# Kernel tuning notes

Hardware: AMD Instinct MI355X
Metric: run time of the kernel (lower is better)

The kernel has to match this reference:

```python
import jax, jax.numpy as jnp
import numpy as np

N_NODES = 50000


def _gcn_conv(x, src, dst, W, b, num_nodes):
    """PyG GCNConv: out = D^{-1/2}(A+I)D^{-1/2} (x @ W) + b, self-loops added."""
    h = x @ W  # [N, out]
    # degrees over edges incl. self-loops (src/dst already include self-loops)
    ones = jnp.ones(src.shape[0], dtype=h.dtype)
    deg = jax.ops.segment_sum(ones, dst, num_segments=num_nodes)
    dinv = jnp.where(deg > 0, jax.lax.rsqrt(deg), 0.0)
    norm = dinv[src] * dinv[dst]  # [E]
    msgs = h[src] * norm[:, None]  # [E, out] gather (memory-bound)
    out = jax.ops.segment_sum(msgs, dst, num_segments=num_nodes)
    return out + b


def setup_inputs() -> dict:
    key = jax.random.key(0)
    ks = jax.random.split(key, 8)
    in_c, h2, h1, out_c = 256, 256, 128, 128
    x = jax.random.normal(ks[0], (N_NODES, in_c), dtype=jnp.float32)
    edge_index = jax.random.randint(ks[1], (2, 800000), 0, N_NODES, dtype=jnp.int64)
    def glorot(k, fi, fo):
        s = float(np.sqrt(6.0 / (fi + fo)))
        return jax.random.uniform(k, (fi, fo), jnp.float32, -s, s)
    return {
        "x": x,
        "edge_index": edge_index,
        "W1": glorot(ks[2], in_c, h2), "b1": jnp.zeros((h2,), jnp.float32),
        "W2": glorot(ks[3], h2, h1), "b2": jnp.zeros((h1,), jnp.float32),
        "W3": glorot(ks[4], h1, out_c), "b3": jnp.zeros((out_c,), jnp.float32),
    }


def reference(x, edge_index, W1, b1, W2, b2, W3, b3):
    n = x.shape[0]
    loops = jnp.arange(n, dtype=edge_index.dtype)
    src = jnp.concatenate([edge_index[0], loops])
    dst = jnp.concatenate([edge_index[1], loops])
    # dropout is a no-op in eval mode (training=False)
    h1 = jax.nn.relu(_gcn_conv(x, src, dst, W1, b1, n))
    h2 = jax.nn.relu(_gcn_conv(h1, src, dst, W2, b2, n))
    h3 = jax.nn.relu(_gcn_conv(h2, src, dst, W3, b3, n))
    return jnp.concatenate([h1, h2, h3], axis=1)
```

## Files before the change

kernel.cpp:

```cpp
#include <hip/hip_runtime.h>

typedef __attribute__((ext_vector_type(8))) short bfrag8;
typedef __attribute__((ext_vector_type(4))) float f32x4v;

__device__ inline short f2bf(float f) {
    unsigned u = __builtin_bit_cast(unsigned, f);
    u = (u + 0x7FFFu + ((u >> 16) & 1u)) >> 16;
    return (short)u;
}
__device__ inline float bf2f(short s) {
    unsigned u = ((unsigned)(unsigned short)s) << 16;
    return __builtin_bit_cast(float, u);
}
__device__ inline int pack2(short lo, short hi) {
    return (int)(((unsigned)(unsigned short)lo) | (((unsigned)(unsigned short)hi) << 16));
}
__device__ inline int pad32i(int v) { return (v + 31) & ~31; }


__global__ void deg_count_kernel(const int* __restrict__ dst, int E, int* __restrict__ deg) {
    int e = blockIdx.x * blockDim.x + threadIdx.x;
    if (e < E) atomicAdd(&deg[dst[e]], 1);
}

__global__ void block_sum_kernel(const int* __restrict__ deg, int n, int* __restrict__ bsums) {
    int i = blockIdx.x * 256 + threadIdx.x;
    int v = (i < n) ? pad32i(deg[i] + 1) : 0;
#pragma unroll
    for (int off = 32; off > 0; off >>= 1) v += __shfl_down(v, off);
    __shared__ int wsum[4];
    int lane = threadIdx.x & 63, w = threadIdx.x >> 6;
    if (lane == 0) wsum[w] = v;
    __syncthreads();
    if (threadIdx.x == 0) bsums[blockIdx.x] = wsum[0] + wsum[1] + wsum[2] + wsum[3];
}

__global__ void scan_bsums_kernel(int* __restrict__ bsums, int B, int* __restrict__ offs, int n) {
    __shared__ int s[256];
    int tid = threadIdx.x;
    int v = (tid < B) ? bsums[tid] : 0;
    s[tid] = v;
    __syncthreads();
    for (int off = 1; off < 256; off <<= 1) {
        int t = (tid >= off) ? s[tid - off] : 0;
        __syncthreads();
        s[tid] += t;
        __syncthreads();
    }
    if (tid < B) bsums[tid] = (tid == 0) ? 0 : s[tid - 1];
    if (tid == 0) offs[n] = s[255];
}

__global__ void scan_final_kernel(const int* __restrict__ deg, int n,
                                  const int* __restrict__ bsums,
                                  int* __restrict__ offs, int* __restrict__ cursor,
                                  float* __restrict__ dinv, int* __restrict__ csr) {
    __shared__ int s[256];
    int tid = threadIdx.x;
    int i = blockIdx.x * 256 + tid;
    int vt = (i < n) ? deg[i] + 1 : 0;
    int pv = (i < n) ? pad32i(vt) : 0;
    s[tid] = pv;
    __syncthreads();
    for (int off = 1; off < 256; off <<= 1) {
        int t = (tid >= off) ? s[tid - off] : 0;
        __syncthreads();
        s[tid] += t;
        __syncthreads();
    }
    if (i < n) {
        int excl = s[tid] - pv + bsums[blockIdx.x];
        offs[i] = excl;
        csr[excl] = i;
        cursor[i] = excl + 1;
        for (int p = excl + vt; p < excl + pv; ++p) csr[p] = n;
        dinv[i] = rsqrtf((float)vt);
    }
}

__global__ void csr_fill_kernel(const int* __restrict__ src, const int* __restrict__ dst, int E,
                                int* __restrict__ cursor, int* __restrict__ csr) {
    int e = blockIdx.x * blockDim.x + threadIdx.x;
    if (e < E) {
        int d = dst[e];
        int p = atomicAdd(&cursor[d], 1);
        csr[p] = src[e];
    }
}


__global__ void prep_kernel(const float* __restrict__ x, short* __restrict__ xb,
                            int total8, int totalp8,
                            const float* __restrict__ W1, short* __restrict__ Wt1,
                            const float* __restrict__ W2, short* __restrict__ Wt2,
                            const float* __restrict__ W3, short* __restrict__ Wt3) {
    int i = blockIdx.x * blockDim.x + threadIdx.x;
    if (i < total8) {
        const float4* p = (const float4*)(x + (size_t)i * 8);
        float4 v0 = p[0], v1 = p[1];
        int4 w = make_int4(pack2(f2bf(v0.x), f2bf(v0.y)), pack2(f2bf(v0.z), f2bf(v0.w)),
                           pack2(f2bf(v1.x), f2bf(v1.y)), pack2(f2bf(v1.z), f2bf(v1.w)));
        *(int4*)(xb + (size_t)i * 8) = w;
    } else if (i < totalp8) {
        *(int4*)(xb + (size_t)i * 8) = make_int4(0, 0, 0, 0);
    } else {
        int j = i - totalp8;
        if (j < 65536) {
            int k = j >> 8, c = j & 255;
            Wt1[c * 256 + k] = f2bf(W1[j]);
        } else if (j < 65536 + 32768) {
            int m = j - 65536;
            int k = m >> 7, c = m & 127;
            Wt2[c * 256 + k] = f2bf(W2[m]);
        } else if (j < 65536 + 32768 + 16384) {
            int m = j - 65536 - 32768;
            int k = m >> 7, c = m & 127;
            Wt3[c * 128 + k] = f2bf(W3[m]);
        }
    }
}


template<int K>
__global__ __launch_bounds__(256, 2) void gemm_skinny_kernel(
        const short* __restrict__ A,
        const short* __restrict__ Bt,
        const float* __restrict__ dinv,
        short* __restrict__ Tout, int ldt) {
    __shared__ short Bs[128 * K];
    char* bsb = (char*)Bs;

    const int tid = threadIdx.x;
    const int lane = tid & 63;
    const int wid = tid >> 6;
    const int l15 = lane & 15;
    const int quad = lane >> 4;
    const int q8 = quad * 8;
    const int bn = blockIdx.y * 128;
    const int row0 = blockIdx.x * 256 + wid * 64;

    {
        constexpr int TOT16 = 128 * K / 8;
#pragma unroll
        for (int i = tid; i < TOT16; i += 256) {
            int r = i / (K / 8);
            int c = (i % (K / 8)) * 8;
            int byte = (r * K + c) * 2;
            byte ^= (r & 7) << 4;
            *(int4*)(bsb + byte) = *(const int4*)&Bt[(size_t)(bn + r) * K + c];
        }
    }
    __syncthreads();

    f32x4v acc[4][8];
#pragma unroll
    for (int i = 0; i < 4; ++i)
#pragma unroll
        for (int j = 0; j < 8; ++j) acc[i][j] = (f32x4v){0.f, 0.f, 0.f, 0.f};

    const short* aBase = A + (size_t)(row0 + l15) * K + q8;

#pragma unroll
    for (int ks = 0; ks < K / 32; ++ks) {
        bfrag8 af[4], bf[8];
#pragma unroll
        for (int mt = 0; mt < 4; ++mt)
            af[mt] = *(const bfrag8*)(aBase + (size_t)mt * 16 * K + ks * 32);
#pragma unroll
        for (int nt = 0; nt < 8; ++nt) {
            int r = nt * 16 + l15;
            int byte = (r * K + ks * 32 + q8) * 2;
            byte ^= (r & 7) << 4;
            bf[nt] = *(const bfrag8*)(bsb + byte);
        }
#pragma unroll
        for (int mt = 0; mt < 4; ++mt)
#pragma unroll
            for (int nt = 0; nt < 8; ++nt)
                acc[mt][nt] = __builtin_amdgcn_mfma_f32_16x16x32_bf16(af[mt], bf[nt], acc[mt][nt], 0, 0, 0);
    }

#pragma unroll
    for (int mt = 0; mt < 4; ++mt) {
#pragma unroll
        for (int r = 0; r < 4; ++r) {
            int grow = row0 + mt * 16 + quad * 4 + r;
            float di = dinv[grow];
            short* outp = Tout + (size_t)grow * ldt + bn + l15;
#pragma unroll
            for (int nt = 0; nt < 8; ++nt)
                outp[nt * 16] = f2bf(acc[mt][nt][r] * di);
        }
    }
}


template<bool WB>
__global__ __launch_bounds__(256) void agg256_kernel(
        const short* __restrict__ hn, const float* __restrict__ dinv,
        const int* __restrict__ offs, const int* __restrict__ csr,
        const float* __restrict__ bias, float* __restrict__ out,
        short* __restrict__ hb, int coloff, int n) {
    int node = blockIdx.x * 4 + (threadIdx.x >> 6);
    if (node >= n) return;
    int lane = threadIdx.x & 63;
    int hl = lane & 31;
    int sub = lane >> 5;
    const short* base = hn + hl * 8;

    float acc[8];
#pragma unroll
    for (int v = 0; v < 8; ++v) acc[v] = 0.f;

    int beg = offs[node], end = offs[node + 1];
    for (int e = beg + sub; e < end; e += 16) {
        int s[8];
#pragma unroll
        for (int j = 0; j < 8; ++j) s[j] = csr[e + 2 * j];
        bfrag8 r[8];
#pragma unroll
        for (int j = 0; j < 8; ++j) r[j] = *(const bfrag8*)(base + (size_t)s[j] * 256);
#pragma unroll
        for (int j = 0; j < 8; ++j)
#pragma unroll
            for (int v = 0; v < 8; ++v) acc[v] += bf2f(r[j][v]);
    }

#pragma unroll
    for (int v = 0; v < 8; ++v) acc[v] += __shfl_xor(acc[v], 32);

    if (sub == 0) {
        float di = dinv[node];
        float res[8];
#pragma unroll
        for (int v = 0; v < 8; ++v)
            res[v] = fmaxf(fmaf(di, acc[v], bias[hl * 8 + v]), 0.f);
        float4* op = (float4*)(out + (size_t)node * 512 + coloff + hl * 8);
        op[0] = make_float4(res[0], res[1], res[2], res[3]);
        op[1] = make_float4(res[4], res[5], res[6], res[7]);
        if (WB) {
            int4 w = make_int4(pack2(f2bf(res[0]), f2bf(res[1])), pack2(f2bf(res[2]), f2bf(res[3])),
                               pack2(f2bf(res[4]), f2bf(res[5])), pack2(f2bf(res[6]), f2bf(res[7])));
            *(int4*)(hb + (size_t)node * 256 + hl * 8) = w;
        }
    }
}


template<bool WB>
__global__ __launch_bounds__(256) void agg128_kernel(
        const short* __restrict__ hn, const float* __restrict__ dinv,
        const int* __restrict__ offs, const int* __restrict__ csr,
        const float* __restrict__ bias, float* __restrict__ out,
        short* __restrict__ hb, int coloff, int n) {
    int node = blockIdx.x * 4 + (threadIdx.x >> 6);
    if (node >= n) return;
    int lane = threadIdx.x & 63;
    int ch = lane & 15;
    int sub = lane >> 4;
    const short* base = hn + ch * 8;

    float acc[8];
#pragma unroll
    for (int v = 0; v < 8; ++v) acc[v] = 0.f;

    int beg = offs[node], end = offs[node + 1];
    for (int e = beg + sub; e < end; e += 32) {
        int s[8];
#pragma unroll
        for (int j = 0; j < 8; ++j) s[j] = csr[e + 4 * j];
        bfrag8 r[8];
#pragma unroll
        for (int j = 0; j < 8; ++j) r[j] = *(const bfrag8*)(base + (size_t)s[j] * 128);
#pragma unroll
        for (int j = 0; j < 8; ++j)
#pragma unroll
            for (int v = 0; v < 8; ++v) acc[v] += bf2f(r[j][v]);
    }

#pragma unroll
    for (int v = 0; v < 8; ++v) {
        acc[v] += __shfl_xor(acc[v], 16);
        acc[v] += __shfl_xor(acc[v], 32);
    }

    if (sub == 0) {
        float di = dinv[node];
        float res[8];
#pragma unroll
        for (int v = 0; v < 8; ++v)
            res[v] = fmaxf(fmaf(di, acc[v], bias[ch * 8 + v]), 0.f);
        float4* op = (float4*)(out + (size_t)node * 512 + coloff + ch * 8);
        op[0] = make_float4(res[0], res[1], res[2], res[3]);
        op[1] = make_float4(res[4], res[5], res[6], res[7]);
        if (WB) {
            int4 w = make_int4(pack2(f2bf(res[0]), f2bf(res[1])), pack2(f2bf(res[2]), f2bf(res[3])),
                               pack2(f2bf(res[4]), f2bf(res[5])), pack2(f2bf(res[6]), f2bf(res[7])));
            *(int4*)(hb + (size_t)node * 128 + ch * 8) = w;
        }
    }
}


extern "C" void kernel_launch(void* const* d_in, const int* in_sizes, int n_in,
                              void* d_out, int out_size, void* d_ws, size_t ws_size,
                              hipStream_t stream) {
    const float* x  = (const float*)d_in[0];
    const int*   ei = (const int*)d_in[1];
    const float* W1 = (const float*)d_in[2];
    const float* b1 = (const float*)d_in[3];
    const float* W2 = (const float*)d_in[4];
    const float* b2 = (const float*)d_in[5];
    const float* W3 = (const float*)d_in[6];
    const float* b3 = (const float*)d_in[7];

    const int IN_C = 256, H2 = 256, H1 = 128, OUT_C = 128;
    int n = in_sizes[0] / IN_C;
    int E = in_sizes[1] / 2;
    const int* src = ei;
    const int* dst = ei + E;

    int sb = (n + 255) / 256;
    int npad = sb * 256;

    char* ws = (char*)d_ws;
    auto carve = [&](size_t bytes) { char* p = ws; ws += (bytes + 255) & ~(size_t)255; return p; };
    int*   deg    = (int*)  carve((size_t)n * 4);
    int*   offs   = (int*)  carve(((size_t)n + 1) * 4);
    int*   cursor = (int*)  carve((size_t)n * 4);
    float* dinv   = (float*)carve((size_t)npad * 4);
    int*   csr    = (int*)  carve(((size_t)E + 32 * (size_t)n) * 4);
    int*   bsums  = (int*)  carve(256 * 4);
    short* Wt1    = (short*)carve((size_t)IN_C * H2 * 2);
    short* Wt2    = (short*)carve((size_t)H2 * H1 * 2);
    short* Wt3    = (short*)carve((size_t)H1 * OUT_C * 2);
    short* t      = (short*)carve((size_t)npad * 256 * 2);
    short* inb    = (short*)carve((size_t)npad * 256 * 2);

    float* out = (float*)d_out;
    int nblk = (n + 255) / 256;

    hipMemsetAsync(deg, 0, (size_t)n * sizeof(int), stream);
    deg_count_kernel<<<(E + 255) / 256, 256, 0, stream>>>(dst, E, deg);
    block_sum_kernel<<<nblk, 256, 0, stream>>>(deg, n, bsums);
    scan_bsums_kernel<<<1, 256, 0, stream>>>(bsums, nblk, offs, n);
    scan_final_kernel<<<nblk, 256, 0, stream>>>(deg, n, bsums, offs, cursor, dinv, csr);
    csr_fill_kernel<<<(E + 255) / 256, 256, 0, stream>>>(src, dst, E, cursor, csr);

    int total8 = n * IN_C / 8;
    int totalp8 = npad * IN_C / 8;
    int prepTot = totalp8 + 65536 + 32768 + 16384;
    prep_kernel<<<(prepTot + 255) / 256, 256, 0, stream>>>(
        x, inb, total8, totalp8, W1, Wt1, W2, Wt2, W3, Wt3);

    gemm_skinny_kernel<256><<<dim3(sb, H2 / 128), 256, 0, stream>>>(inb, Wt1, dinv, t, H2);
    agg256_kernel<true><<<(n + 3) / 4, 256, 0, stream>>>(t, dinv, offs, csr, b1, out, inb, 0, n);

    gemm_skinny_kernel<256><<<dim3(sb, H1 / 128), 256, 0, stream>>>(inb, Wt2, dinv, t, H1);
    agg128_kernel<true><<<(n + 3) / 4, 256, 0, stream>>>(t, dinv, offs, csr, b2, out, inb, H2, n);

    hipMemsetAsync(inb + (size_t)n * 128, 0, (size_t)(npad - n) * 128 * 2, stream);

    gemm_skinny_kernel<128><<<dim3(sb, OUT_C / 128), 256, 0, stream>>>(inb, Wt3, dinv, t, OUT_C);
    agg128_kernel<false><<<(n + 3) / 4, 256, 0, stream>>>(t, dinv, offs, csr, b3, out, nullptr, H2 + H1, n);
}
```

Measured before the change: 425.5 us.

## Halve CSR row padding, vectorize atomics, fuse scans, add nontemporal memory ops

CSR rows are now padded to multiples of 16 instead of 32. This cuts the dummy gathers in aggregation, and agg128 gets a half-width tail iteration to cover rows that are not multiples of 32. The degree-count and CSR-fill kernels each process four edges per thread with int4 loads. The block-sum scan is folded into scan_final so one launch disappears. The separate padding memset is replaced by having agg128 zero the padded rows. Index loads and output stores now use nontemporal hints, which may change cache behaviour for data that is reused.

```diff
diff --git a/kernel.cpp b/kernel.cpp
--- a/kernel.cpp
+++ b/kernel.cpp
@@ -2,6 +2,7 @@
 
 typedef __attribute__((ext_vector_type(8))) short bfrag8;
 typedef __attribute__((ext_vector_type(4))) float f32x4v;
+typedef __attribute__((ext_vector_type(4))) int   i32x4v;
 
 __device__ inline short f2bf(float f) {
     unsigned u = __builtin_bit_cast(unsigned, f);
@@ -15,17 +16,23 @@
 __device__ inline int pack2(short lo, short hi) {
     return (int)(((unsigned)(unsigned short)lo) | (((unsigned)(unsigned short)hi) << 16));
 }
-__device__ inline int pad32i(int v) { return (v + 31) & ~31; }
+__device__ inline int pad16i(int v) { return (v + 15) & ~15; }
 
 
 __global__ void deg_count_kernel(const int* __restrict__ dst, int E, int* __restrict__ deg) {
-    int e = blockIdx.x * blockDim.x + threadIdx.x;
-    if (e < E) atomicAdd(&deg[dst[e]], 1);
+    int e = (blockIdx.x * blockDim.x + threadIdx.x) * 4;
+    if (e + 3 < E) {
+        int4 d = *(const int4*)(dst + e);
+        atomicAdd(&deg[d.x], 1); atomicAdd(&deg[d.y], 1);
+        atomicAdd(&deg[d.z], 1); atomicAdd(&deg[d.w], 1);
+    } else {
+        for (; e < E; ++e) atomicAdd(&deg[dst[e]], 1);
+    }
 }
 
 __global__ void block_sum_kernel(const int* __restrict__ deg, int n, int* __restrict__ bsums) {
     int i = blockIdx.x * 256 + threadIdx.x;
-    int v = (i < n) ? pad32i(deg[i] + 1) : 0;
+    int v = (i < n) ? pad16i(deg[i] + 1) : 0;
 #pragma unroll
     for (int off = 32; off > 0; off >>= 1) v += __shfl_down(v, off);
     __shared__ int wsum[4];
@@ -35,31 +42,26 @@
     if (threadIdx.x == 0) bsums[blockIdx.x] = wsum[0] + wsum[1] + wsum[2] + wsum[3];
 }
 
-__global__ void scan_bsums_kernel(int* __restrict__ bsums, int B, int* __restrict__ offs, int n) {
-    __shared__ int s[256];
-    int tid = threadIdx.x;
-    int v = (tid < B) ? bsums[tid] : 0;
-    s[tid] = v;
-    __syncthreads();
-    for (int off = 1; off < 256; off <<= 1) {
-        int t = (tid >= off) ? s[tid - off] : 0;
-        __syncthreads();
-        s[tid] += t;
-        __syncthreads();
-    }
-    if (tid < B) bsums[tid] = (tid == 0) ? 0 : s[tid - 1];
-    if (tid == 0) offs[n] = s[255];
-}
-
-__global__ void scan_final_kernel(const int* __restrict__ deg, int n,
+__global__ void scan_final_kernel(const int* __restrict__ deg, int n, int B,
                                   const int* __restrict__ bsums,
                                   int* __restrict__ offs, int* __restrict__ cursor,
                                   float* __restrict__ dinv, int* __restrict__ csr) {
+    __shared__ int sb[256];
     __shared__ int s[256];
     int tid = threadIdx.x;
+    sb[tid] = (tid < B) ? bsums[tid] : 0;
+    __syncthreads();
+    for (int off = 1; off < 256; off <<= 1) {
+        int t = (tid >= off) ? sb[tid - off] : 0;
+        __syncthreads();
+        sb[tid] += t;
+        __syncthreads();
+    }
+    int myBase = (blockIdx.x == 0) ? 0 : sb[blockIdx.x - 1];
+    int total = sb[255];
     int i = blockIdx.x * 256 + tid;
     int vt = (i < n) ? deg[i] + 1 : 0;
-    int pv = (i < n) ? pad32i(vt) : 0;
+    int pv = (i < n) ? pad16i(vt) : 0;
     s[tid] = pv;
     __syncthreads();
     for (int off = 1; off < 256; off <<= 1) {
@@ -69,22 +71,35 @@
         __syncthreads();
     }
     if (i < n) {
-        int excl = s[tid] - pv + bsums[blockIdx.x];
+        int excl = s[tid] - pv + myBase;
         offs[i] = excl;
         csr[excl] = i;
         cursor[i] = excl + 1;
         for (int p = excl + vt; p < excl + pv; ++p) csr[p] = n;
         dinv[i] = rsqrtf((float)vt);
-    }
+    } else if (i < gridDim.x * 256) {
+        dinv[i] = 0.f;
+    }
+    if (blockIdx.x == 0 && tid == 0) offs[n] = total;
 }
 
 __global__ void csr_fill_kernel(const int* __restrict__ src, const int* __restrict__ dst, int E,
                                 int* __restrict__ cursor, int* __restrict__ csr) {
-    int e = blockIdx.x * blockDim.x + threadIdx.x;
-    if (e < E) {
-        int d = dst[e];
-        int p = atomicAdd(&cursor[d], 1);
-        csr[p] = src[e];
+    int e = (blockIdx.x * blockDim.x + threadIdx.x) * 4;
+    if (e + 3 < E) {
+        int4 s4 = *(const int4*)(src + e);
+        int4 d4 = *(const int4*)(dst + e);
+        int p;
+        p = atomicAdd(&cursor[d4.x], 1); __builtin_nontemporal_store(s4.x, csr + p);
+        p = atomicAdd(&cursor[d4.y], 1); __builtin_nontemporal_store(s4.y, csr + p);
+        p = atomicAdd(&cursor[d4.z], 1); __builtin_nontemporal_store(s4.z, csr + p);
+        p = atomicAdd(&cursor[d4.w], 1); __builtin_nontemporal_store(s4.w, csr + p);
+    } else {
+        for (; e < E; ++e) {
+            int d = dst[e];
+            int p = atomicAdd(&cursor[d], 1);
+            __builtin_nontemporal_store(src[e], csr + p);
+        }
     }
 }
 
@@ -216,7 +231,7 @@
     for (int e = beg + sub; e < end; e += 16) {
         int s[8];
 #pragma unroll
-        for (int j = 0; j < 8; ++j) s[j] = csr[e + 2 * j];
+        for (int j = 0; j < 8; ++j) s[j] = __builtin_nontemporal_load(csr + e + 2 * j);
         bfrag8 r[8];
 #pragma unroll
         for (int j = 0; j < 8; ++j) r[j] = *(const bfrag8*)(base + (size_t)s[j] * 256);
@@ -235,13 +250,15 @@
 #pragma unroll
         for (int v = 0; v < 8; ++v)
             res[v] = fmaxf(fmaf(di, acc[v], bias[hl * 8 + v]), 0.f);
-        float4* op = (float4*)(out + (size_t)node * 512 + coloff + hl * 8);
-        op[0] = make_float4(res[0], res[1], res[2], res[3]);
-        op[1] = make_float4(res[4], res[5], res[6], res[7]);
+        float* op = out + (size_t)node * 512 + coloff + hl * 8;
+        f32x4v w0 = {res[0], res[1], res[2], res[3]};
+        f32x4v w1 = {res[4], res[5], res[6], res[7]};
+        __builtin_nontemporal_store(w0, (f32x4v*)op);
+        __builtin_nontemporal_store(w1, (f32x4v*)(op + 4));
         if (WB) {
-            int4 w = make_int4(pack2(f2bf(res[0]), f2bf(res[1])), pack2(f2bf(res[2]), f2bf(res[3])),
-                               pack2(f2bf(res[4]), f2bf(res[5])), pack2(f2bf(res[6]), f2bf(res[7])));
-            *(int4*)(hb + (size_t)node * 256 + hl * 8) = w;
+            i32x4v w = {pack2(f2bf(res[0]), f2bf(res[1])), pack2(f2bf(res[2]), f2bf(res[3])),
+                        pack2(f2bf(res[4]), f2bf(res[5])), pack2(f2bf(res[6]), f2bf(res[7]))};
+            __builtin_nontemporal_store(w, (i32x4v*)(hb + (size_t)node * 256 + hl * 8));
         }
     }
 }
@@ -252,10 +269,13 @@
         const short* __restrict__ hn, const float* __restrict__ dinv,
         const int* __restrict__ offs, const int* __restrict__ csr,
         const float* __restrict__ bias, float* __restrict__ out,
-        short* __restrict__ hb, int coloff, int n) {
+        short* __restrict__ hb, int coloff, int n, int npad) {
     int node = blockIdx.x * 4 + (threadIdx.x >> 6);
-    if (node >= n) return;
     int lane = threadIdx.x & 63;
+    if (node >= n) {
+        if (WB && node < npad) ((int*)(hb + (size_t)node * 128))[lane] = 0;
+        return;
+    }
     int ch = lane & 15;
     int sub = lane >> 4;
     const short* base = hn + ch * 8;
@@ -265,15 +285,28 @@
     for (int v = 0; v < 8; ++v) acc[v] = 0.f;
 
     int beg = offs[node], end = offs[node + 1];
-    for (int e = beg + sub; e < end; e += 32) {
+    int e = beg + sub;
+    for (; e + 16 < end; e += 32) {
         int s[8];
 #pragma unroll
-        for (int j = 0; j < 8; ++j) s[j] = csr[e + 4 * j];
+        for (int j = 0; j < 8; ++j) s[j] = __builtin_nontemporal_load(csr + e + 4 * j);
         bfrag8 r[8];
 #pragma unroll
         for (int j = 0; j < 8; ++j) r[j] = *(const bfrag8*)(base + (size_t)s[j] * 128);
 #pragma unroll
         for (int j = 0; j < 8; ++j)
+#pragma unroll
+            for (int v = 0; v < 8; ++v) acc[v] += bf2f(r[j][v]);
+    }
+    if (e < end) {
+        int s[4];
+#pragma unroll
+        for (int j = 0; j < 4; ++j) s[j] = __builtin_nontemporal_load(csr + e + 4 * j);
+        bfrag8 r[4];
+#pragma unroll
+        for (int j = 0; j < 4; ++j) r[j] = *(const bfrag8*)(base + (size_t)s[j] * 128);
+#pragma unroll
+        for (int j = 0; j < 4; ++j)
 #pragma unroll
             for (int v = 0; v < 8; ++v) acc[v] += bf2f(r[j][v]);
     }
@@ -290,13 +323,15 @@
 #pragma unroll
         for (int v = 0; v < 8; ++v)
             res[v] = fmaxf(fmaf(di, acc[v], bias[ch * 8 + v]), 0.f);
-        float4* op = (float4*)(out + (size_t)node * 512 + coloff + ch * 8);
-        op[0] = make_float4(res[0], res[1], res[2], res[3]);
-        op[1] = make_float4(res[4], res[5], res[6], res[7]);
+        float* op = out + (size_t)node * 512 + coloff + ch * 8;
+        f32x4v w0 = {res[0], res[1], res[2], res[3]};
+        f32x4v w1 = {res[4], res[5], res[6], res[7]};
+        __builtin_nontemporal_store(w0, (f32x4v*)op);
+        __builtin_nontemporal_store(w1, (f32x4v*)(op + 4));
         if (WB) {
-            int4 w = make_int4(pack2(f2bf(res[0]), f2bf(res[1])), pack2(f2bf(res[2]), f2bf(res[3])),
-                               pack2(f2bf(res[4]), f2bf(res[5])), pack2(f2bf(res[6]), f2bf(res[7])));
-            *(int4*)(hb + (size_t)node * 128 + ch * 8) = w;
+            i32x4v w = {pack2(f2bf(res[0]), f2bf(res[1])), pack2(f2bf(res[2]), f2bf(res[3])),
+                        pack2(f2bf(res[4]), f2bf(res[5])), pack2(f2bf(res[6]), f2bf(res[7]))};
+            __builtin_nontemporal_store(w, (i32x4v*)(hb + (size_t)node * 128 + ch * 8));
         }
     }
 }
@@ -329,7 +364,7 @@
     int*   offs   = (int*)  carve(((size_t)n + 1) * 4);
     int*   cursor = (int*)  carve((size_t)n * 4);
     float* dinv   = (float*)carve((size_t)npad * 4);
-    int*   csr    = (int*)  carve(((size_t)E + 32 * (size_t)n) * 4);
+    int*   csr    = (int*)  carve(((size_t)E + 16 * (size_t)n) * 4);
     int*   bsums  = (int*)  carve(256 * 4);
     short* Wt1    = (short*)carve((size_t)IN_C * H2 * 2);
     short* Wt2    = (short*)carve((size_t)H2 * H1 * 2);
@@ -341,11 +376,10 @@
     int nblk = (n + 255) / 256;
 
     hipMemsetAsync(deg, 0, (size_t)n * sizeof(int), stream);
-    deg_count_kernel<<<(E + 255) / 256, 256, 0, stream>>>(dst, E, deg);
+    deg_count_kernel<<<(E / 4 + 255) / 256, 256, 0, stream>>>(dst, E, deg);
     block_sum_kernel<<<nblk, 256, 0, stream>>>(deg, n, bsums);
-    scan_bsums_kernel<<<1, 256, 0, stream>>>(bsums, nblk, offs, n);
-    scan_final_kernel<<<nblk, 256, 0, stream>>>(deg, n, bsums, offs, cursor, dinv, csr);
-    csr_fill_kernel<<<(E + 255) / 256, 256, 0, stream>>>(src, dst, E, cursor, csr);
+    scan_final_kernel<<<nblk, 256, 0, stream>>>(deg, n, nblk, bsums, offs, cursor, dinv, csr);
+    csr_fill_kernel<<<(E / 4 + 255) / 256, 256, 0, stream>>>(src, dst, E, cursor, csr);
 
     int total8 = n * IN_C / 8;
     int totalp8 = npad * IN_C / 8;
@@ -357,10 +391,8 @@
     agg256_kernel<true><<<(n + 3) / 4, 256, 0, stream>>>(t, dinv, offs, csr, b1, out, inb, 0, n);
 
     gemm_skinny_kernel<256><<<dim3(sb, H1 / 128), 256, 0, stream>>>(inb, Wt2, dinv, t, H1);
-    agg128_kernel<true><<<(n + 3) / 4, 256, 0, stream>>>(t, dinv, offs, csr, b2, out, inb, H2, n);
-
-    hipMemsetAsync(inb + (size_t)n * 128, 0, (size_t)(npad - n) * 128 * 2, stream);
+    agg128_kernel<true><<<(npad + 3) / 4, 256, 0, stream>>>(t, dinv, offs, csr, b2, out, inb, H2, n, npad);
 
     gemm_skinny_kernel<128><<<dim3(sb, OUT_C / 128), 256, 0, stream>>>(inb, Wt3, dinv, t, OUT_C);
-    agg128_kernel<false><<<(n + 3) / 4, 256, 0, stream>>>(t, dinv, offs, csr, b3, out, nullptr, H2 + H1, n);
-}
+    agg128_kernel<false><<<(n + 3) / 4, 256, 0, stream>>>(t, dinv, offs, csr, b3, out, nullptr, H2 + H1, n, npad);
+}
```

After: 441.7 us. 3.8% more time.
